# Performance work log

Hardware: AMD Instinct MI355X
Metric: run time of the kernel (lower is better)

Reference implementation:

```python
import math
import jax
import jax.numpy as jnp
import numpy as np

DECAY_RATE = 0.99
LOG_CLAMP_MIN = -10.0


def setup_inputs() -> dict:
    key = jax.random.key(0)
    k0, k1, k2, k3, k4, k5 = jax.random.split(key, 6)
    B, S, D, N = 32, 4096, 256, 64
    return {
        "query": jax.random.normal(k0, (B, S, D), dtype=jnp.float32),
        "memory": jax.random.normal(k1, (1, N, D), dtype=jnp.float32),
        "importance": jax.random.uniform(k2, (1, N), dtype=jnp.float32),
        "age": jax.random.uniform(k3, (1, N), dtype=jnp.float32) * 10.0,
        # torch.nn.Linear weights are [out_features, in_features]; applied as x @ W.T
        "W_q": jax.random.normal(k4, (D, D), dtype=jnp.float32) / jnp.sqrt(D).astype(jnp.float32),
        "W_k": jax.random.normal(k5, (D, D), dtype=jnp.float32) / jnp.sqrt(D).astype(jnp.float32),
        "top_k": 8,
    }


def reference(query, memory, importance, age, W_q, W_k, top_k):
    # MemoryBank.read(): top-k masked attention over a small memory bank
    # query: [B, S, D]; memory: [1, N, D]; importance/age: [1, N]
    D = query.shape[-1]
    N = memory.shape[1]
    mem = memory[0]          # [N, D] (buffer is batch-broadcast in torch via expand)

    q = query @ W_q.T                      # [B, S, D]
    k = mem @ W_k.T                        # [N, D]
    scores = jnp.einsum("bsd,nd->bsn", q, k) / jnp.sqrt(jnp.asarray(D, query.dtype))

    # importance-decay bias, log-clamped at -10
    eff_imp = importance[0] * (DECAY_RATE ** age[0])           # [N]
    scores = scores + jnp.maximum(jnp.log(eff_imp), LOG_CLAMP_MIN)[None, None, :]

    if top_k < N:
        _, topk_idx = jax.lax.top_k(scores, top_k)             # [B, S, k]
        # scatter 1.0 at top-k indices (N is small, one-hot sum is cheap)
        mask = jax.nn.one_hot(topk_idx, N, dtype=scores.dtype).sum(axis=-2)  # [B, S, N]
        scores = jnp.where(mask > 0, scores, -jnp.inf)

    attn_weights = jax.nn.softmax(scores, axis=-1)             # [B, S, N]
    retrieved = jnp.einsum("bsn,nd->bsd", attn_weights, mem)   # [B, S, D]
    return retrieved, attn_weights
```

## Files before the change

### kernel.cpp

```cpp
#include <hip/hip_runtime.h>
#include <hip/hip_bf16.h>

#define DD 256
#define NM 64

typedef unsigned long long u64;
typedef float v2f __attribute__((ext_vector_type(2)));

struct v2x2 { v2f lo, hi; };
static __device__ __forceinline__ v2x2 splitf4(float4 f) {
    union { float4 a; v2x2 b; } u; u.a = f; return u.b;
}

#define PK_FMA_SPLATLO(acc, q2, c2) \
    asm("v_pk_fma_f32 %0, %1, %2, %0 op_sel:[0,0,0] op_sel_hi:[0,1,1]" \
        : "+v"(acc) : "v"(q2), "v"(c2))
#define PK_FMA_SPLATHI(acc, q2, c2) \
    asm("v_pk_fma_f32 %0, %1, %2, %0 op_sel:[1,0,0] op_sel_hi:[1,1,1]" \
        : "+v"(acc) : "v"(q2), "v"(c2))

__global__ __launch_bounds__(256) void prep_tr(
    const float* __restrict__ Wq, const float* __restrict__ Wk,
    float* __restrict__ wqt, float* __restrict__ wkt)
{
    const int o = blockIdx.x;
    const int d = threadIdx.x;
    if (blockIdx.y == 0) wqt[d * DD + o] = Wq[o * DD + d];
    else                 wkt[d * DD + o] = Wk[o * DD + d];
}

__global__ __launch_bounds__(256) void prep_kT(
    const float* __restrict__ mem, const float* __restrict__ wkt,
    const float* __restrict__ imp, const float* __restrict__ age,
    float* __restrict__ kT4, float* __restrict__ bias)
{
    const int n = blockIdx.x;
    const int o = threadIdx.x;
    const float* mrow = mem + n * DD;
    float acc = 0.f;
    for (int d = 0; d < DD; ++d)
        acc = fmaf(mrow[d], wkt[d * DD + o], acc);
    kT4[(o >> 2) * (NM * 4) + n * 4 + (o & 3)] = acc;

    if (o == 0) {
        double eff = (double)imp[n] * pow(0.99, (double)age[n]);
        float b = (float)log(eff);
        if (!(b >= -10.0f)) b = -10.0f;
        bias[n] = b;
    }
}

__global__ __launch_bounds__(256, 2) void qgemm4(
    const float* __restrict__ query,
    const float4* __restrict__ wqt4,
    float* __restrict__ qout,
    int M)
{
    __shared__ float q_lds[32 * DD];
    __shared__ float wq_lds[2][8 * 256];

    const int t = threadIdx.x;
    const int l = t & 63;
    const int w = __builtin_amdgcn_readfirstlane((int)(t >> 6));
    const int row0 = blockIdx.x * 32;

    {
        const float4* q4g = reinterpret_cast<const float4*>(query);
#pragma unroll
        for (int i = 0; i < 8; ++i) {
            const int idx = i * 256 + t;
            const int r = idx >> 6, c4 = idx & 63;
            int gr = row0 + r; if (gr > M - 1) gr = M - 1;
            *reinterpret_cast<float4*>(&q_lds[r * DD + c4 * 4]) =
                q4g[(size_t)gr * 64 + c4];
        }
    }
    {
        const float4 s0 = wqt4[t];
        const float4 s1 = wqt4[256 + t];
        reinterpret_cast<float4*>(wq_lds[0])[t]       = s0;
        reinterpret_cast<float4*>(wq_lds[0])[256 + t] = s1;
    }
    __syncthreads();

    v2f a01[8], a23[8];
#pragma unroll
    for (int rr = 0; rr < 8; ++rr) { a01[rr] = (v2f)(0.f); a23[rr] = (v2f)(0.f); }

    const float* qbase = &q_lds[(w * 8) * DD];

    for (int c = 0; c < 32; ++c) {
        const int cn = (c + 1) & 31;
        const float4 n0 = wqt4[cn * 512 + t];
        const float4 n1 = wqt4[cn * 512 + 256 + t];

        {
            const float4* wb = reinterpret_cast<const float4*>(wq_lds[c & 1]);
            float4 cw[8];
#pragma unroll
            for (int i = 0; i < 8; ++i) cw[i] = wb[i * 64 + l];
            const v2x2 c0 = splitf4(cw[0]), c1 = splitf4(cw[1]);
            const v2x2 c2 = splitf4(cw[2]), c3 = splitf4(cw[3]);
            const v2x2 c4 = splitf4(cw[4]), c5 = splitf4(cw[5]);
            const v2x2 c6 = splitf4(cw[6]), c7 = splitf4(cw[7]);
#pragma unroll
            for (int rr = 0; rr < 8; ++rr) {
                const float4 qqA = *reinterpret_cast<const float4*>(
                    qbase + rr * DD + c * 8);
                const float4 qqB = *reinterpret_cast<const float4*>(
                    qbase + rr * DD + c * 8 + 4);
                const v2x2 qA = splitf4(qqA);
                const v2x2 qB = splitf4(qqB);
                PK_FMA_SPLATLO(a01[rr], qA.lo, c0.lo);
                PK_FMA_SPLATLO(a23[rr], qA.lo, c0.hi);
                PK_FMA_SPLATHI(a01[rr], qA.lo, c1.lo);
                PK_FMA_SPLATHI(a23[rr], qA.lo, c1.hi);
                PK_FMA_SPLATLO(a01[rr], qA.hi, c2.lo);
                PK_FMA_SPLATLO(a23[rr], qA.hi, c2.hi);
                PK_FMA_SPLATHI(a01[rr], qA.hi, c3.lo);
                PK_FMA_SPLATHI(a23[rr], qA.hi, c3.hi);
                PK_FMA_SPLATLO(a01[rr], qB.lo, c4.lo);
                PK_FMA_SPLATLO(a23[rr], qB.lo, c4.hi);
                PK_FMA_SPLATHI(a01[rr], qB.lo, c5.lo);
                PK_FMA_SPLATHI(a23[rr], qB.lo, c5.hi);
                PK_FMA_SPLATLO(a01[rr], qB.hi, c6.lo);
                PK_FMA_SPLATLO(a23[rr], qB.hi, c6.hi);
                PK_FMA_SPLATHI(a01[rr], qB.hi, c7.lo);
                PK_FMA_SPLATHI(a23[rr], qB.hi, c7.hi);
            }
        }
        {
            float4* dst = reinterpret_cast<float4*>(wq_lds[(c + 1) & 1]);
            dst[t]       = n0;
            dst[256 + t] = n1;
        }
        __syncthreads();
    }

#pragma unroll
    for (int rr = 0; rr < 8; ++rr) {
        const int grow = row0 + w * 8 + rr;
        if (grow < M) {
            float4 v; v.x = a01[rr].x; v.y = a01[rr].y; v.z = a23[rr].x; v.w = a23[rr].y;
            *reinterpret_cast<float4*>(&qout[(size_t)grow * DD + 4 * l]) = v;
        }
    }
}

__global__ __launch_bounds__(256, 2) void scores_k(
    const float* __restrict__ qin,
    const float4* __restrict__ kT44,
    const float* __restrict__ bias,
    float* __restrict__ sout,
    int M)
{
    __shared__ float q_lds[32 * DD];
    const int t = threadIdx.x;
    const int l = t & 63;
    const int w = __builtin_amdgcn_readfirstlane((int)(t >> 6));
    const int row0 = blockIdx.x * 32;

    {
        const float4* q4g = reinterpret_cast<const float4*>(qin);
#pragma unroll
        for (int i = 0; i < 8; ++i) {
            const int idx = i * 256 + t;
            const int r = idx >> 6, c4 = idx & 63;
            int gr = row0 + r; if (gr > M - 1) gr = M - 1;
            *reinterpret_cast<float4*>(&q_lds[r * DD + c4 * 4]) =
                q4g[(size_t)gr * 64 + c4];
        }
    }
    __syncthreads();

    const int n = l;
    const float bn = bias[n];
    float sc[8];
#pragma unroll
    for (int r = 0; r < 8; ++r) sc[r] = 0.f;

    const float* qbase = &q_lds[(w * 8) * DD];
    for (int og = 0; og < DD / 4; ++og) {
        const float4 kt = kT44[og * NM + n];
#pragma unroll
        for (int r = 0; r < 8; ++r) {
            const float4 q4 = *reinterpret_cast<const float4*>(
                qbase + r * DD + og * 4);
            float v = sc[r];
            v = fmaf(q4.x, kt.x, v);
            v = fmaf(q4.y, kt.y, v);
            v = fmaf(q4.z, kt.z, v);
            v = fmaf(q4.w, kt.w, v);
            sc[r] = v;
        }
    }
#pragma unroll
    for (int r = 0; r < 8; ++r) {
        const int grow = row0 + w * 8 + r;
        if (grow < M) sout[(size_t)grow * NM + n] = sc[r] * 0.0625f + bn;
    }
}

#define FR 128
__global__ __launch_bounds__(256, 2) void fin3(
    const float* __restrict__ mem,
    const int* __restrict__ topk_p,
    float* __restrict__ out_ret,
    float* __restrict__ out_attn,
    int M)
{
    __shared__ float s_lds[FR * NM];
    __shared__ int   sel_i[FR * 16];
    __shared__ float sel_w[FR * 16];

    const int t = threadIdx.x;
    const int l = t & 63;
    const int w = __builtin_amdgcn_readfirstlane((int)(t >> 6));
    const int row0 = blockIdx.x * FR;
    const int k = *topk_p;

    {
#pragma unroll
        for (int i = 0; i < (FR * NM / 4) / 256; ++i) {
            const int idx = i * 256 + t;
            const int r = idx >> 4, c4 = idx & 15;
            int gr = row0 + r; if (gr > M - 1) gr = M - 1;
            const float4 v = *reinterpret_cast<const float4*>(
                &out_attn[(size_t)gr * NM + c4 * 4]);
            s_lds[r * NM + ((c4 * 4 + 0 + r) & 63)] = v.x;
            s_lds[r * NM + ((c4 * 4 + 1 + r) & 63)] = v.y;
            s_lds[r * NM + ((c4 * 4 + 2 + r) & 63)] = v.z;
            s_lds[r * NM + ((c4 * 4 + 3 + r) & 63)] = v.w;
        }
    }
    __syncthreads();

    if (t < FR) {
        const int r = t;
        float sv[NM];
#pragma unroll
        for (int n = 0; n < NM; ++n) sv[n] = s_lds[r * NM + ((n + r) & 63)];

        if (k < NM) {
            const int kk = k < 16 ? k : 16;
            u64 taken = 0ull;
            float mmax = 0.f, Z = 0.f;
            for (int i = 0; i < kk; ++i) {
                float m = -1.0e30f;
                int idx = 0;
#pragma unroll
                for (int n = 0; n < NM; ++n) {
                    const bool avail  = ((taken >> n) & 1ull) == 0ull;
                    const bool better = avail && (sv[n] > m);
                    m   = better ? sv[n] : m;
                    idx = better ? n : idx;
                }
                taken |= (1ull << idx);
                if (i == 0) mmax = m;
                const float wv = expf(m - mmax);
                Z += wv;
                sel_i[r * 16 + i] = idx;
                sel_w[r * 16 + i] = wv;
            }
#pragma unroll
            for (int n = 0; n < NM; ++n) s_lds[r * NM + ((n + r) & 63)] = 0.f;
            for (int i = 0; i < kk; ++i) {
                const float wz = sel_w[r * 16 + i] / Z;
                sel_w[r * 16 + i] = wz;
                s_lds[r * NM + ((sel_i[r * 16 + i] + r) & 63)] = wz;
            }
        } else {
            float m = -1.0e30f;
#pragma unroll
            for (int n = 0; n < NM; ++n) m = sv[n] > m ? sv[n] : m;
            float Z = 0.f;
#pragma unroll
            for (int n = 0; n < NM; ++n) Z += expf(sv[n] - m);
#pragma unroll
            for (int n = 0; n < NM; ++n) s_lds[r * NM + ((n + r) & 63)] = expf(sv[n] - m) / Z;
        }
    }
    __syncthreads();

#pragma unroll
    for (int i = 0; i < (FR * NM) / 256; ++i) {
        const int idx = i * 256 + t;
        const int r = idx >> 6, n = idx & 63;
        const int grow = row0 + r;
        if (grow < M) out_attn[(size_t)grow * NM + n] = s_lds[r * NM + ((n + r) & 63)];
    }

    {
        const float4* mem4 = reinterpret_cast<const float4*>(mem);
        const int kk = k < 16 ? k : 16;
#pragma unroll 1
        for (int rr = 0; rr < FR / 4; ++rr) {
            const int r    = w * (FR / 4) + rr;
            const int grow = row0 + r;
            if (grow >= M) continue;
            float4 acc; acc.x = 0.f; acc.y = 0.f; acc.z = 0.f; acc.w = 0.f;
            if (k < NM) {
                for (int i = 0; i < kk; ++i) {
                    const int   mi = sel_i[r * 16 + i];
                    const float wz = sel_w[r * 16 + i];
                    const float4 mv = mem4[mi * 64 + l];
                    acc.x = fmaf(wz, mv.x, acc.x);
                    acc.y = fmaf(wz, mv.y, acc.y);
                    acc.z = fmaf(wz, mv.z, acc.z);
                    acc.w = fmaf(wz, mv.w, acc.w);
                }
            } else {
                for (int n = 0; n < NM; ++n) {
                    const float wz = s_lds[r * NM + ((n + r) & 63)];
                    const float4 mv = mem4[n * 64 + l];
                    acc.x = fmaf(wz, mv.x, acc.x);
                    acc.y = fmaf(wz, mv.y, acc.y);
                    acc.z = fmaf(wz, mv.z, acc.z);
                    acc.w = fmaf(wz, mv.w, acc.w);
                }
            }
            *reinterpret_cast<float4*>(&out_ret[(size_t)grow * DD + 4 * l]) = acc;
        }
    }
}

extern "C" void kernel_launch(void* const* d_in, const int* in_sizes, int n_in,
                              void* d_out, int out_size, void* d_ws, size_t ws_size,
                              hipStream_t stream) {
    const float* query      = (const float*)d_in[0];
    const float* memory     = (const float*)d_in[1];
    const float* importance = (const float*)d_in[2];
    const float* age        = (const float*)d_in[3];
    const float* Wq         = (const float*)d_in[4];
    const float* Wk         = (const float*)d_in[5];
    const int*   topk       = (const int*)d_in[6];

    const int M = in_sizes[0] / DD;

    float* kT4  = (float*)d_ws;
    float* bias = kT4 + (size_t)DD * NM;
    float* wqt  = bias + 64;
    float* wkt  = wqt + (size_t)DD * DD;

    hipLaunchKernelGGL(prep_tr, dim3(DD, 2), dim3(DD), 0, stream,
                       Wq, Wk, wqt, wkt);
    hipLaunchKernelGGL(prep_kT, dim3(NM), dim3(DD), 0, stream,
                       memory, wkt, importance, age, kT4, bias);

    float* out_ret  = (float*)d_out;
    float* out_attn = out_ret + (size_t)M * DD;

    hipLaunchKernelGGL(qgemm4, dim3((M + 31) / 32), dim3(256), 0, stream,
                       query, (const float4*)wqt, out_ret, M);
    hipLaunchKernelGGL(scores_k, dim3((M + 31) / 32), dim3(256), 0, stream,
                       out_ret, (const float4*)kT4, bias, out_attn, M);
    hipLaunchKernelGGL(fin3, dim3((M + FR - 1) / FR), dim3(256), 0, stream,
                       memory, topk, out_ret, out_attn, M);
}
```

Baseline: 398.2 us.

## Fuse score computation with top-k softmax and retrieval kernel

Merges the scores kernel and the top-k/softmax/retrieval kernel into one kernel working on 32-row tiles. Scores stay in LDS instead of going to global memory and being read back, and one kernel launch is removed. In exchange only 32 of 256 threads do the serial top-k selection per block, the tile is smaller than the previous 128 rows, and LDS use per block rises, which may lower occupancy. The retrieved output overwrites the q buffer (out_ret) that other blocks read, but each block reads only its own rows before writing them.

```diff
diff --git a/kernel.cpp b/kernel.cpp
--- a/kernel.cpp
+++ b/kernel.cpp
@@ -147,18 +147,26 @@
     }
 }
 
-__global__ __launch_bounds__(256, 2) void scores_k(
+__global__ __launch_bounds__(256, 2) void sfin(
     const float* __restrict__ qin,
+    const float* __restrict__ mem,
     const float4* __restrict__ kT44,
     const float* __restrict__ bias,
-    float* __restrict__ sout,
+    const int* __restrict__ topk_p,
+    float* __restrict__ out_ret,
+    float* __restrict__ out_attn,
     int M)
 {
     __shared__ float q_lds[32 * DD];
+    __shared__ float s_lds[32 * NM];
+    __shared__ int   sel_i[32 * 16];
+    __shared__ float sel_w[32 * 16];
+
     const int t = threadIdx.x;
     const int l = t & 63;
     const int w = __builtin_amdgcn_readfirstlane((int)(t >> 6));
     const int row0 = blockIdx.x * 32;
+    const int k = *topk_p;
 
     {
         const float4* q4g = reinterpret_cast<const float4*>(qin);
@@ -173,69 +181,37 @@
     }
     __syncthreads();
 
-    const int n = l;
-    const float bn = bias[n];
-    float sc[8];
-#pragma unroll
-    for (int r = 0; r < 8; ++r) sc[r] = 0.f;
-
-    const float* qbase = &q_lds[(w * 8) * DD];
-    for (int og = 0; og < DD / 4; ++og) {
-        const float4 kt = kT44[og * NM + n];
+    {
+        const int n = l;
+        const float bn = bias[n];
+        float sc[8];
+#pragma unroll
+        for (int r = 0; r < 8; ++r) sc[r] = 0.f;
+
+        const float* qbase = &q_lds[(w * 8) * DD];
+        for (int og = 0; og < DD / 4; ++og) {
+            const float4 kt = kT44[og * NM + n];
+#pragma unroll
+            for (int r = 0; r < 8; ++r) {
+                const float4 q4 = *reinterpret_cast<const float4*>(
+                    qbase + r * DD + og * 4);
+                float v = sc[r];
+                v = fmaf(q4.x, kt.x, v);
+                v = fmaf(q4.y, kt.y, v);
+                v = fmaf(q4.z, kt.z, v);
+                v = fmaf(q4.w, kt.w, v);
+                sc[r] = v;
+            }
+        }
 #pragma unroll
         for (int r = 0; r < 8; ++r) {
-            const float4 q4 = *reinterpret_cast<const float4*>(
-                qbase + r * DD + og * 4);
-            float v = sc[r];
-            v = fmaf(q4.x, kt.x, v);
-            v = fmaf(q4.y, kt.y, v);
-            v = fmaf(q4.z, kt.z, v);
-            v = fmaf(q4.w, kt.w, v);
-            sc[r] = v;
-        }
-    }
-#pragma unroll
-    for (int r = 0; r < 8; ++r) {
-        const int grow = row0 + w * 8 + r;
-        if (grow < M) sout[(size_t)grow * NM + n] = sc[r] * 0.0625f + bn;
-    }
-}
-
-#define FR 128
-__global__ __launch_bounds__(256, 2) void fin3(
-    const float* __restrict__ mem,
-    const int* __restrict__ topk_p,
-    float* __restrict__ out_ret,
-    float* __restrict__ out_attn,
-    int M)
-{
-    __shared__ float s_lds[FR * NM];
-    __shared__ int   sel_i[FR * 16];
-    __shared__ float sel_w[FR * 16];
-
-    const int t = threadIdx.x;
-    const int l = t & 63;
-    const int w = __builtin_amdgcn_readfirstlane((int)(t >> 6));
-    const int row0 = blockIdx.x * FR;
-    const int k = *topk_p;
-
-    {
-#pragma unroll
-        for (int i = 0; i < (FR * NM / 4) / 256; ++i) {
-            const int idx = i * 256 + t;
-            const int r = idx >> 4, c4 = idx & 15;
-            int gr = row0 + r; if (gr > M - 1) gr = M - 1;
-            const float4 v = *reinterpret_cast<const float4*>(
-                &out_attn[(size_t)gr * NM + c4 * 4]);
-            s_lds[r * NM + ((c4 * 4 + 0 + r) & 63)] = v.x;
-            s_lds[r * NM + ((c4 * 4 + 1 + r) & 63)] = v.y;
-            s_lds[r * NM + ((c4 * 4 + 2 + r) & 63)] = v.z;
-            s_lds[r * NM + ((c4 * 4 + 3 + r) & 63)] = v.w;
+            const int gr = w * 8 + r;
+            s_lds[gr * NM + ((n + gr) & 63)] = sc[r] * 0.0625f + bn;
         }
     }
     __syncthreads();
 
-    if (t < FR) {
+    if (t < 32) {
         const int r = t;
         float sv[NM];
 #pragma unroll
@@ -283,7 +259,7 @@
     __syncthreads();
 
 #pragma unroll
-    for (int i = 0; i < (FR * NM) / 256; ++i) {
+    for (int i = 0; i < 8; ++i) {
         const int idx = i * 256 + t;
         const int r = idx >> 6, n = idx & 63;
         const int grow = row0 + r;
@@ -294,8 +270,8 @@
         const float4* mem4 = reinterpret_cast<const float4*>(mem);
         const int kk = k < 16 ? k : 16;
 #pragma unroll 1
-        for (int rr = 0; rr < FR / 4; ++rr) {
-            const int r    = w * (FR / 4) + rr;
+        for (int rr = 0; rr < 8; ++rr) {
+            const int r    = w * 8 + rr;
             const int grow = row0 + r;
             if (grow >= M) continue;
             float4 acc; acc.x = 0.f; acc.y = 0.f; acc.z = 0.f; acc.w = 0.f;
@@ -352,8 +328,7 @@
 
     hipLaunchKernelGGL(qgemm4, dim3((M + 31) / 32), dim3(256), 0, stream,
                        query, (const float4*)wqt, out_ret, M);
-    hipLaunchKernelGGL(scores_k, dim3((M + 31) / 32), dim3(256), 0, stream,
-                       out_ret, (const float4*)kT4, bias, out_attn, M);
-    hipLaunchKernelGGL(fin3, dim3((M + FR - 1) / FR), dim3(256), 0, stream,
-                       memory, topk, out_ret, out_attn, M);
-}
+    hipLaunchKernelGGL(sfin, dim3((M + 31) / 32), dim3(256), 0, stream,
+                       out_ret, memory, (const float4*)kT4, bias, topk,
+                       out_ret, out_attn, M);
+}
```

Result: slower. 462.2 us (+16.1%).

## Fuse query projection GEMM with score computation through LDS

Applied to the files above, without the earlier changes.

Merges the q projection kernel and the scores kernel into one. The projected q tile is written back into shared memory and then dotted with the key matrix in place, so q no longer makes a round trip through global memory (a write of M×256 floats and a read back). The price is a longer kernel with extra LDS traffic and an added barrier. Register pressure may also rise, which could lower occupancy.

```diff
diff --git a/kernel.cpp b/kernel.cpp
--- a/kernel.cpp
+++ b/kernel.cpp
@@ -50,10 +50,12 @@
     }
 }
 
-__global__ __launch_bounds__(256, 2) void qgemm4(
+__global__ __launch_bounds__(256, 2) void qgemm_s(
     const float* __restrict__ query,
     const float4* __restrict__ wqt4,
-    float* __restrict__ qout,
+    const float4* __restrict__ kT44,
+    const float* __restrict__ bias,
+    float* __restrict__ sout,
     int M)
 {
     __shared__ float q_lds[32 * DD];
@@ -87,117 +89,93 @@
 #pragma unroll
     for (int rr = 0; rr < 8; ++rr) { a01[rr] = (v2f)(0.f); a23[rr] = (v2f)(0.f); }
 
-    const float* qbase = &q_lds[(w * 8) * DD];
-
-    for (int c = 0; c < 32; ++c) {
-        const int cn = (c + 1) & 31;
-        const float4 n0 = wqt4[cn * 512 + t];
-        const float4 n1 = wqt4[cn * 512 + 256 + t];
-
-        {
-            const float4* wb = reinterpret_cast<const float4*>(wq_lds[c & 1]);
-            float4 cw[8];
-#pragma unroll
-            for (int i = 0; i < 8; ++i) cw[i] = wb[i * 64 + l];
-            const v2x2 c0 = splitf4(cw[0]), c1 = splitf4(cw[1]);
-            const v2x2 c2 = splitf4(cw[2]), c3 = splitf4(cw[3]);
-            const v2x2 c4 = splitf4(cw[4]), c5 = splitf4(cw[5]);
-            const v2x2 c6 = splitf4(cw[6]), c7 = splitf4(cw[7]);
-#pragma unroll
-            for (int rr = 0; rr < 8; ++rr) {
-                const float4 qqA = *reinterpret_cast<const float4*>(
-                    qbase + rr * DD + c * 8);
-                const float4 qqB = *reinterpret_cast<const float4*>(
-                    qbase + rr * DD + c * 8 + 4);
-                const v2x2 qA = splitf4(qqA);
-                const v2x2 qB = splitf4(qqB);
-                PK_FMA_SPLATLO(a01[rr], qA.lo, c0.lo);
-                PK_FMA_SPLATLO(a23[rr], qA.lo, c0.hi);
-                PK_FMA_SPLATHI(a01[rr], qA.lo, c1.lo);
-                PK_FMA_SPLATHI(a23[rr], qA.lo, c1.hi);
-                PK_FMA_SPLATLO(a01[rr], qA.hi, c2.lo);
-                PK_FMA_SPLATLO(a23[rr], qA.hi, c2.hi);
-                PK_FMA_SPLATHI(a01[rr], qA.hi, c3.lo);
-                PK_FMA_SPLATHI(a23[rr], qA.hi, c3.hi);
-                PK_FMA_SPLATLO(a01[rr], qB.lo, c4.lo);
-                PK_FMA_SPLATLO(a23[rr], qB.lo, c4.hi);
-                PK_FMA_SPLATHI(a01[rr], qB.lo, c5.lo);
-                PK_FMA_SPLATHI(a23[rr], qB.lo, c5.hi);
-                PK_FMA_SPLATLO(a01[rr], qB.hi, c6.lo);
-                PK_FMA_SPLATLO(a23[rr], qB.hi, c6.hi);
-                PK_FMA_SPLATHI(a01[rr], qB.hi, c7.lo);
-                PK_FMA_SPLATHI(a23[rr], qB.hi, c7.hi);
-            }
-        }
-        {
-            float4* dst = reinterpret_cast<float4*>(wq_lds[(c + 1) & 1]);
-            dst[t]       = n0;
-            dst[256 + t] = n1;
-        }
-        __syncthreads();
+    {
+        const float* qbase = &q_lds[(w * 8) * DD];
+
+        for (int c = 0; c < 32; ++c) {
+            const int cn = (c + 1) & 31;
+            const float4 n0 = wqt4[cn * 512 + t];
+            const float4 n1 = wqt4[cn * 512 + 256 + t];
+
+            {
+                const float4* wb = reinterpret_cast<const float4*>(wq_lds[c & 1]);
+                float4 cw[8];
+#pragma unroll
+                for (int i = 0; i < 8; ++i) cw[i] = wb[i * 64 + l];
+                const v2x2 c0 = splitf4(cw[0]), c1 = splitf4(cw[1]);
+                const v2x2 c2 = splitf4(cw[2]), c3 = splitf4(cw[3]);
+                const v2x2 c4 = splitf4(cw[4]), c5 = splitf4(cw[5]);
+                const v2x2 c6 = splitf4(cw[6]), c7 = splitf4(cw[7]);
+#pragma unroll
+                for (int rr = 0; rr < 8; ++rr) {
+                    const float4 qqA = *reinterpret_cast<const float4*>(
+                        qbase + rr * DD + c * 8);
+                    const float4 qqB = *reinterpret_cast<const float4*>(
+                        qbase + rr * DD + c * 8 + 4);
+                    const v2x2 qA = splitf4(qqA);
+                    const v2x2 qB = splitf4(qqB);
+                    PK_FMA_SPLATLO(a01[rr], qA.lo, c0.lo);
+                    PK_FMA_SPLATLO(a23[rr], qA.lo, c0.hi);
+                    PK_FMA_SPLATHI(a01[rr], qA.lo, c1.lo);
+                    PK_FMA_SPLATHI(a23[rr], qA.lo, c1.hi);
+                    PK_FMA_SPLATLO(a01[rr], qA.hi, c2.lo);
+                    PK_FMA_SPLATLO(a23[rr], qA.hi, c2.hi);
+                    PK_FMA_SPLATHI(a01[rr], qA.hi, c3.lo);
+                    PK_FMA_SPLATHI(a23[rr], qA.hi, c3.hi);
+                    PK_FMA_SPLATLO(a01[rr], qB.lo, c4.lo);
+                    PK_FMA_SPLATLO(a23[rr], qB.lo, c4.hi);
+                    PK_FMA_SPLATHI(a01[rr], qB.lo, c5.lo);
+                    PK_FMA_SPLATHI(a23[rr], qB.lo, c5.hi);
+                    PK_FMA_SPLATLO(a01[rr], qB.hi, c6.lo);
+                    PK_FMA_SPLATLO(a23[rr], qB.hi, c6.hi);
+                    PK_FMA_SPLATHI(a01[rr], qB.hi, c7.lo);
+                    PK_FMA_SPLATHI(a23[rr], qB.hi, c7.hi);
+                }
+            }
+            {
+                float4* dst = reinterpret_cast<float4*>(wq_lds[(c + 1) & 1]);
+                dst[t]       = n0;
+                dst[256 + t] = n1;
+            }
+            __syncthreads();
+        }
     }
 
 #pragma unroll
     for (int rr = 0; rr < 8; ++rr) {
-        const int grow = row0 + w * 8 + rr;
-        if (grow < M) {
-            float4 v; v.x = a01[rr].x; v.y = a01[rr].y; v.z = a23[rr].x; v.w = a23[rr].y;
-            *reinterpret_cast<float4*>(&qout[(size_t)grow * DD + 4 * l]) = v;
-        }
-    }
-}
-
-__global__ __launch_bounds__(256, 2) void scores_k(
-    const float* __restrict__ qin,
-    const float4* __restrict__ kT44,
-    const float* __restrict__ bias,
-    float* __restrict__ sout,
-    int M)
-{
-    __shared__ float q_lds[32 * DD];
-    const int t = threadIdx.x;
-    const int l = t & 63;
-    const int w = __builtin_amdgcn_readfirstlane((int)(t >> 6));
-    const int row0 = blockIdx.x * 32;
-
-    {
-        const float4* q4g = reinterpret_cast<const float4*>(qin);
-#pragma unroll
-        for (int i = 0; i < 8; ++i) {
-            const int idx = i * 256 + t;
-            const int r = idx >> 6, c4 = idx & 63;
-            int gr = row0 + r; if (gr > M - 1) gr = M - 1;
-            *reinterpret_cast<float4*>(&q_lds[r * DD + c4 * 4]) =
-                q4g[(size_t)gr * 64 + c4];
-        }
+        const int lr = w * 8 + rr;
+        float4 v; v.x = a01[rr].x; v.y = a01[rr].y; v.z = a23[rr].x; v.w = a23[rr].y;
+        *reinterpret_cast<float4*>(&q_lds[lr * DD + 4 * l]) = v;
     }
     __syncthreads();
 
-    const int n = l;
-    const float bn = bias[n];
-    float sc[8];
-#pragma unroll
-    for (int r = 0; r < 8; ++r) sc[r] = 0.f;
-
-    const float* qbase = &q_lds[(w * 8) * DD];
-    for (int og = 0; og < DD / 4; ++og) {
-        const float4 kt = kT44[og * NM + n];
+    {
+        const int n = l;
+        const float bn = bias[n];
+        float sc[8];
+#pragma unroll
+        for (int r = 0; r < 8; ++r) sc[r] = 0.f;
+
+        const float* qbase = &q_lds[(w * 8) * DD];
+        for (int og = 0; og < DD / 4; ++og) {
+            const float4 kt = kT44[og * NM + n];
+#pragma unroll
+            for (int r = 0; r < 8; ++r) {
+                const float4 q4 = *reinterpret_cast<const float4*>(
+                    qbase + r * DD + og * 4);
+                float v = sc[r];
+                v = fmaf(q4.x, kt.x, v);
+                v = fmaf(q4.y, kt.y, v);
+                v = fmaf(q4.z, kt.z, v);
+                v = fmaf(q4.w, kt.w, v);
+                sc[r] = v;
+            }
+        }
 #pragma unroll
         for (int r = 0; r < 8; ++r) {
-            const float4 q4 = *reinterpret_cast<const float4*>(
-                qbase + r * DD + og * 4);
-            float v = sc[r];
-            v = fmaf(q4.x, kt.x, v);
-            v = fmaf(q4.y, kt.y, v);
-            v = fmaf(q4.z, kt.z, v);
-            v = fmaf(q4.w, kt.w, v);
-            sc[r] = v;
-        }
-    }
-#pragma unroll
-    for (int r = 0; r < 8; ++r) {
-        const int grow = row0 + w * 8 + r;
-        if (grow < M) sout[(size_t)grow * NM + n] = sc[r] * 0.0625f + bn;
+            const int grow = row0 + w * 8 + r;
+            if (grow < M) sout[(size_t)grow * NM + n] = sc[r] * 0.0625f + bn;
+        }
     }
 }
 
@@ -350,10 +328,9 @@
     float* out_ret  = (float*)d_out;
     float* out_attn = out_ret + (size_t)M * DD;
 
-    hipLaunchKernelGGL(qgemm4, dim3((M + 31) / 32), dim3(256), 0, stream,
-                       query, (const float4*)wqt, out_ret, M);
-    hipLaunchKernelGGL(scores_k, dim3((M + 31) / 32), dim3(256), 0, stream,
-                       out_ret, (const float4*)kT4, bias, out_attn, M);
+    hipLaunchKernelGGL(qgemm_s, dim3((M + 31) / 32), dim3(256), 0, stream,
+                       query, (const float4*)wqt, (const float4*)kT4,
+                       bias, out_attn, M);
     hipLaunchKernelGGL(fin3, dim3((M + FR - 1) / FR), dim3(256), 0, stream,
                        memory, topk, out_ret, out_attn, M);
 }
```

Result: no change. 400.1 us (+0.5%).

## Remap scores kernel so lanes own rows and broadcast K tiles

Applied to the files above, without the earlier changes.

The scores kernel now uses 512-thread blocks covering 64 rows, with each lane owning one query row and each wave owning 8 memory slots. Previously each lane owned one memory slot and read query rows from LDS. Now K^T values are wave-uniform loads (broadcast/scalar-friendly), and query rows are read from an XOR-swizzled LDS layout to avoid bank conflicts. Results are transposed through LDS with a rotated layout so the global stores stay coalesced. The cost is an extra LDS round trip and barriers, plus higher LDS use per block, which may limit occupancy.

```diff
diff --git a/kernel.cpp b/kernel.cpp
--- a/kernel.cpp
+++ b/kernel.cpp
@@ -147,57 +147,66 @@
     }
 }
 
-__global__ __launch_bounds__(256, 2) void scores_k(
+__global__ __launch_bounds__(512, 2) void scores_b(
     const float* __restrict__ qin,
     const float4* __restrict__ kT44,
     const float* __restrict__ bias,
     float* __restrict__ sout,
     int M)
 {
-    __shared__ float q_lds[32 * DD];
+    __shared__ float q_lds[64 * DD];
     const int t = threadIdx.x;
     const int l = t & 63;
     const int w = __builtin_amdgcn_readfirstlane((int)(t >> 6));
-    const int row0 = blockIdx.x * 32;
+    const int row0 = blockIdx.x * 64;
 
     {
         const float4* q4g = reinterpret_cast<const float4*>(qin);
 #pragma unroll
         for (int i = 0; i < 8; ++i) {
-            const int idx = i * 256 + t;
+            const int idx = i * 512 + t;
             const int r = idx >> 6, c4 = idx & 63;
             int gr = row0 + r; if (gr > M - 1) gr = M - 1;
-            *reinterpret_cast<float4*>(&q_lds[r * DD + c4 * 4]) =
+            *reinterpret_cast<float4*>(&q_lds[r * DD + ((c4 ^ r) & 63) * 4]) =
                 q4g[(size_t)gr * 64 + c4];
         }
     }
     __syncthreads();
 
-    const int n = l;
-    const float bn = bias[n];
+    const int nb = w * 8;
     float sc[8];
 #pragma unroll
-    for (int r = 0; r < 8; ++r) sc[r] = 0.f;
-
-    const float* qbase = &q_lds[(w * 8) * DD];
+    for (int j = 0; j < 8; ++j) sc[j] = 0.f;
+
     for (int og = 0; og < DD / 4; ++og) {
-        const float4 kt = kT44[og * NM + n];
-#pragma unroll
-        for (int r = 0; r < 8; ++r) {
-            const float4 q4 = *reinterpret_cast<const float4*>(
-                qbase + r * DD + og * 4);
-            float v = sc[r];
+        const float4 q4 = *reinterpret_cast<const float4*>(
+            &q_lds[l * DD + (((og ^ l) & 63) << 2)]);
+        const float4* ktp = kT44 + og * NM + nb;
+#pragma unroll
+        for (int j = 0; j < 8; ++j) {
+            const float4 kt = ktp[j];
+            float v = sc[j];
             v = fmaf(q4.x, kt.x, v);
             v = fmaf(q4.y, kt.y, v);
             v = fmaf(q4.z, kt.z, v);
             v = fmaf(q4.w, kt.w, v);
-            sc[r] = v;
-        }
-    }
-#pragma unroll
-    for (int r = 0; r < 8; ++r) {
-        const int grow = row0 + w * 8 + r;
-        if (grow < M) sout[(size_t)grow * NM + n] = sc[r] * 0.0625f + bn;
+            sc[j] = v;
+        }
+    }
+    __syncthreads();
+
+    float* s_tmp = q_lds;
+#pragma unroll
+    for (int j = 0; j < 8; ++j)
+        s_tmp[l * NM + ((nb + j + l) & 63)] = sc[j] * 0.0625f + bias[nb + j];
+    __syncthreads();
+
+#pragma unroll
+    for (int i = 0; i < 8; ++i) {
+        const int idx = i * 512 + t;
+        const int r = idx >> 6, n = idx & 63;
+        const int grow = row0 + r;
+        if (grow < M) sout[(size_t)grow * NM + n] = s_tmp[r * NM + ((n + r) & 63)];
     }
 }
 
@@ -352,7 +361,7 @@
 
     hipLaunchKernelGGL(qgemm4, dim3((M + 31) / 32), dim3(256), 0, stream,
                        query, (const float4*)wqt, out_ret, M);
-    hipLaunchKernelGGL(scores_k, dim3((M + 31) / 32), dim3(256), 0, stream,
+    hipLaunchKernelGGL(scores_b, dim3((M + 63) / 64), dim3(512), 0, stream,
                        out_ret, (const float4*)kT4, bias, out_attn, M);
     hipLaunchKernelGGL(fin3, dim3((M + FR - 1) / FR), dim3(256), 0, stream,
                        memory, topk, out_ret, out_attn, M);
```

Result: no change. 397.1 us (-0.3%).
